# Kernel optimization log

Measured on AMD Instinct MI355X. Metric: run time of the kernel, lower is better.

Reference implementation:

```python
import jax, jax.numpy as jnp
import numpy as np

N = 32768      # nodes
H = 128        # hidden_channels
G = 50         # num_gaussians
F = 128        # num_filters
E = 524288     # edges (avg degree 16)
CUTOFF = 10.0
LOG2 = np.float32(np.log(2.0))


def _lin_init(key, fan_in, fan_out):
    return (jax.random.normal(key, (fan_in, fan_out), jnp.float32) / jnp.sqrt(jnp.float32(fan_in)))


def setup_inputs() -> dict:
    key = jax.random.key(0)
    ks = jax.random.split(key, 12)
    h = jax.random.normal(ks[0], (N, H), jnp.float32)
    pos = jax.random.uniform(ks[1], (N, 3), jnp.float32, minval=0.0, maxval=10.0)
    edge_index = jax.random.randint(ks[2], (2, E), 0, N, jnp.int32)
    virtual_edge_mask = jax.random.randint(ks[3], (E,), 0, 2, jnp.int32) == 1
    return {
        "h": h, "pos": pos,
        "edge_index": edge_index, "virtual_edge_mask": virtual_edge_mask,
        # attn_mlp: Linear(2H+G, H) -> ReLU -> Linear(H, 1)
        "attn_w1": _lin_init(ks[4], 2 * H + G, H), "attn_b1": jnp.zeros((H,), jnp.float32),
        "attn_w2": _lin_init(ks[5], H, 1), "attn_b2": jnp.zeros((1,), jnp.float32),
        # CFConv filter mlp: Linear(G, F) -> ssp -> Linear(F, F)
        "filt_w1": _lin_init(ks[6], G, F), "filt_b1": jnp.zeros((F,), jnp.float32),
        "filt_w2": _lin_init(ks[7], F, F), "filt_b2": jnp.zeros((F,), jnp.float32),
        # CFConv lin1 (no bias), lin2; InteractionBlock output lin
        "lin1_w": _lin_init(ks[8], H, F),
        "lin2_w": _lin_init(ks[9], F, H), "lin2_b": jnp.zeros((H,), jnp.float32),
        "lin_w": _lin_init(ks[10], H, H), "lin_b": jnp.zeros((H,), jnp.float32),
    }


def _ssp(x):  # ShiftedSoftplus
    return jax.nn.softplus(x) - LOG2


def _gaussian_smearing(d):  # [E] -> [E, G]
    offset = jnp.linspace(0.0, CUTOFF, G, dtype=jnp.float32)
    coeff = -0.5 / (offset[1] - offset[0]) ** 2
    return jnp.exp(coeff * (d[:, None] - offset) ** 2)


def _masked_scatter_softmax(score, seg, mask):
    # softmax of score over edges grouped by seg, restricted to mask; 1.0 elsewhere
    neg = jnp.where(mask, score, -jnp.inf)
    m = jax.ops.segment_max(neg, seg, num_segments=N)
    m = jnp.where(jnp.isfinite(m), m, 0.0)
    e = jnp.where(mask, jnp.exp(score - m[seg]), 0.0)
    s = jax.ops.segment_sum(e, seg, num_segments=N)
    return jnp.where(mask, e / (s[seg] + 1e-16), 1.0)


def reference(h, pos, edge_index, virtual_edge_mask,
              attn_w1, attn_b1, attn_w2, attn_b2,
              filt_w1, filt_b1, filt_w2, filt_b2,
              lin1_w, lin2_w, lin2_b, lin_w, lin_b):
    row, col = edge_index[0], edge_index[1]
    d = jnp.linalg.norm(pos[row] - pos[col], axis=-1)          # [E]
    edge_attr = _gaussian_smearing(d)                          # [E, G]

    # attention score over cat(h_i, h_j, edge_attr)
    feat = jnp.concatenate([h[row], h[col], edge_attr], axis=-1)   # [E, 2H+G]
    score = (jax.nn.relu(feat @ attn_w1 + attn_b1) @ attn_w2 + attn_b2)[:, 0]  # [E]
    decay = _masked_scatter_softmax(score, row, virtual_edge_mask)  # [E]
    edge_attr = edge_attr * decay[:, None]

    # PyG SchNet InteractionBlock / CFConv
    C = 0.5 * (jnp.cos(d * jnp.float32(np.pi) / CUTOFF) + 1.0)     # [E]
    W = (_ssp(edge_attr @ filt_w1 + filt_b1) @ filt_w2 + filt_b2) * C[:, None]  # [E, F]
    x = h @ lin1_w                                                  # [N, F]
    msg = x[row] * W                                                # [E, F]
    agg = jax.ops.segment_sum(msg, col, num_segments=N)             # [N, F]
    x = agg @ lin2_w + lin2_b
    h_update = _ssp(x) @ lin_w + lin_b                              # [N, H]
    return h_update, pos
```

## Files before the change

### kernel.cpp

```cpp
#include <hip/hip_runtime.h>

#define NN 32768
#define HH 128
#define GG 50
#define EE 524288

constexpr float GSTEP = 10.0f / 49.0f;
constexpr float GCOEF = -0.5f / (GSTEP * GSTEP);
constexpr float PI_OVER_CUT = 0.31415926535897931f;
constexpr float LOG2F_ = 0.69314718055994531f;
constexpr float LOG2E_ = 1.4426950408889634f;
constexpr float RLOG2E_ = 0.69314718055994531f;
constexpr float GC2 = GCOEF * LOG2E_;

typedef __attribute__((ext_vector_type(8))) short bf16x8;
typedef __attribute__((ext_vector_type(4))) float f32x4;
typedef unsigned short ushort_t;

__device__ __forceinline__ float fast_exp2(float x) {
    float r; asm("v_exp_f32 %0, %1" : "=v"(r) : "v"(x)); return r;
}
__device__ __forceinline__ float fast_log2(float x) {
    float r; asm("v_log_f32 %0, %1" : "=v"(r) : "v"(x)); return r;
}
__device__ __forceinline__ float fexpf(float x) {
    return fast_exp2(x * LOG2E_);
}
__device__ __forceinline__ float sspf(float x) {
    const float p = fast_exp2(x * LOG2E_);
    const float r = RLOG2E_ * fast_log2(1.0f + p) - LOG2F_;
    return (x > 80.0f) ? (x - LOG2F_) : r;
}
__device__ __forceinline__ unsigned fenc(float f) {
    unsigned b = __float_as_uint(f);
    return (b & 0x80000000u) ? ~b : (b | 0x80000000u);
}
__device__ __forceinline__ float fdec(unsigned u) {
    unsigned b = (u & 0x80000000u) ? (u ^ 0x80000000u) : ~u;
    return __uint_as_float(b);
}
__device__ __forceinline__ int get_mask(const void* mp, int mode, int e) {
    if (mode) return ((const unsigned char*)mp)[e] != 0;
    return ((const int*)mp)[e] != 0;
}
__device__ __forceinline__ ushort_t f2bf(float f) {
    unsigned u = __float_as_uint(f);
    return (ushort_t)((u + 0x7FFFu + ((u >> 16) & 1u)) >> 16);
}
__device__ __forceinline__ float bf2f(ushort_t s) { return __uint_as_float(((unsigned)s) << 16); }

__global__ void k_detect(const unsigned char* __restrict__ mb, int* __restrict__ flag) {
    __shared__ int any;
    if (threadIdx.x == 0) any = 0;
    __syncthreads();
    int local = 0;
    for (int i = threadIdx.x; i < 16384; i += blockDim.x)
        if ((i & 3) != 0 && mb[i]) local = 1;
    if (local) atomicOr(&any, 1);
    __syncthreads();
    if (threadIdx.x == 0) *flag = any;
}

__global__ void k_prep_w(const float* __restrict__ filt_w1, const float* __restrict__ filt_w2,
                         const float* __restrict__ attn_w1, const float* __restrict__ lin1_w,
                         const float* __restrict__ lin2_w, const float* __restrict__ lin_w,
                         ushort_t* __restrict__ w1t, ushort_t* __restrict__ w1ct,
                         ushort_t* __restrict__ w2t, ushort_t* __restrict__ wut,
                         ushort_t* __restrict__ wvt, ushort_t* __restrict__ wxt,
                         ushort_t* __restrict__ l2t, ushort_t* __restrict__ lwt)
{
    const int t = blockIdx.x * 256 + threadIdx.x;
    if (t < 8192) {
        const int n = t >> 6, g = t & 63;
        w1t[t] = f2bf((g < GG) ? filt_w1[g * HH + n] : 0.0f);
    } else if (t < 16384) {
        const int i = t - 8192, n = i >> 6, g = i & 63;
        w1ct[i] = f2bf((g < GG) ? attn_w1[(size_t)(256 + g) * HH + n] : 0.0f);
    } else if (t < 32768) {
        const int i = t - 16384, n = i >> 7, k = i & 127;
        w2t[i] = f2bf(filt_w2[k * HH + n]);
    } else if (t < 49152) {
        const int i = t - 32768, n = i >> 7, k = i & 127;
        wut[i] = f2bf(attn_w1[(size_t)k * HH + n]);
    } else if (t < 65536) {
        const int i = t - 49152, n = i >> 7, k = i & 127;
        wvt[i] = f2bf(attn_w1[(size_t)(128 + k) * HH + n]);
    } else if (t < 81920) {
        const int i = t - 65536, n = i >> 7, k = i & 127;
        wxt[i] = f2bf(lin1_w[(size_t)k * HH + n]);
    } else if (t < 98304) {
        const int i = t - 81920, n = i >> 7, k = i & 127;
        l2t[i] = f2bf(lin2_w[(size_t)k * HH + n]);
    } else if (t < 114688) {
        const int i = t - 98304, n = i >> 7, k = i & 127;
        lwt[i] = f2bf(lin_w[(size_t)k * HH + n]);
    }
}

__global__ __launch_bounds__(256, 4) void k_node_proj(
    const float* __restrict__ h,
    const ushort_t* __restrict__ wut, const ushort_t* __restrict__ wvt,
    const ushort_t* __restrict__ wxt,
    ushort_t* __restrict__ ub, ushort_t* __restrict__ vb, ushort_t* __restrict__ xhb)
{
    __shared__ alignas(16) unsigned char smem[32768];
    unsigned char* HB = smem;
    unsigned char* WB = smem + 16384;

    const int tid = threadIdx.x;
    const int n0 = blockIdx.x * 64;
    const int mat = blockIdx.y;
    const ushort_t* __restrict__ wt = (mat == 0) ? wut : (mat == 1 ? wvt : wxt);
    ushort_t* __restrict__ out = (mat == 0) ? ub : (mat == 1 ? vb : xhb);

    for (int p = tid; p < 2048; p += 256) {
        const int row = p >> 5, c4 = p & 31;
        const float4 v = *(const float4*)(h + (size_t)(n0 + row) * HH + c4 * 4);
        uint2 pk = {(unsigned)f2bf(v.x) | ((unsigned)f2bf(v.y) << 16),
                    (unsigned)f2bf(v.z) | ((unsigned)f2bf(v.w) << 16)};
        const int lbyte = row * 256 + c4 * 8;
        *(uint2*)(HB + (lbyte ^ ((row & 7) << 4))) = pk;
    }
    for (int p = tid; p < 1024; p += 256) {
        const int byte = p * 16; const int nl = byte >> 8;
        *(float4*)(WB + (byte ^ ((nl & 7) << 4))) = *(const float4*)((const char*)wt + byte);
    }
    __syncthreads();

    const int lane = tid & 63, wv = tid >> 6, col0 = lane & 15, g4 = lane >> 4;
    const int m = wv * 16 + col0;
    f32x4 acc[8] = {};
#pragma unroll
    for (int hh2 = 0; hh2 < 2; hh2++) {
        if (hh2 == 1) {
            __syncthreads();
            for (int p = tid; p < 1024; p += 256) {
                const int byte = p * 16; const int nl = byte >> 8;
                *(float4*)(WB + (byte ^ ((nl & 7) << 4))) =
                    *(const float4*)((const char*)wt + 16384 + byte);
            }
            __syncthreads();
        }
#pragma unroll
        for (int kk = 0; kk < 4; kk++) {
            const int abyte = m * 256 + kk * 64 + g4 * 16;
            const bf16x8 af = *(const bf16x8*)(HB + (abyte ^ ((m & 7) << 4)));
#pragma unroll
            for (int q = 0; q < 4; q++) {
                const int l = q * 16 + col0;
                const int bbyte = l * 256 + kk * 64 + g4 * 16;
                const bf16x8 bf_ = *(const bf16x8*)(WB + (bbyte ^ ((l & 7) << 4)));
                acc[hh2 * 4 + q] = __builtin_amdgcn_mfma_f32_16x16x32_bf16(af, bf_, acc[hh2 * 4 + q], 0, 0, 0);
            }
        }
    }
#pragma unroll
    for (int f = 0; f < 8; f++) {
        const int col = (f >> 2) * 64 + (f & 3) * 16 + col0;
#pragma unroll
        for (int rg = 0; rg < 4; rg++) {
            const int row = wv * 16 + g4 * 4 + rg;
            out[(size_t)(n0 + row) * HH + col] = f2bf(acc[f][rg]);
        }
    }
}

__global__ __launch_bounds__(256, 4) void k_edge_score(
    const float* __restrict__ pos, const int* __restrict__ ei,
    const void* __restrict__ maskp, const int* __restrict__ flagp,
    const ushort_t* __restrict__ ub, const ushort_t* __restrict__ vb,
    const ushort_t* __restrict__ w1ct, const float* __restrict__ attn_b1,
    const float* __restrict__ attn_w2, const float* __restrict__ attn_b2,
    float* __restrict__ dbuf, float* __restrict__ score, unsigned* __restrict__ menc,
    int* __restrict__ count)
{
    __shared__ alignas(16) unsigned char EA[8192];
    __shared__ alignas(16) unsigned char WC[16384];
    __shared__ float dsh[64];
    __shared__ int rsh[64], csh[64];

    const int tid  = threadIdx.x;
    const int e0   = blockIdx.x * 64;
    const int lane = tid & 63;
    const int wv   = tid >> 6;
    const int col0 = lane & 15;
    const int g4   = lane >> 4;

    if (tid < 64) {
        const int e = e0 + tid;
        const int r = ei[e], c = ei[EE + e];
        rsh[tid] = r; csh[tid] = c;
        atomicAdd(&count[c], 1);
        const float dx = pos[r * 3 + 0] - pos[c * 3 + 0];
        const float dy = pos[r * 3 + 1] - pos[c * 3 + 1];
        const float dz = pos[r * 3 + 2] - pos[c * 3 + 2];
        const float d = sqrtf(dx * dx + dy * dy + dz * dz);
        dsh[tid] = d;
        dbuf[e] = d;
    }
    for (int p = tid; p < 1024; p += 256) {
        const int byte = p * 16;
        const int n = byte >> 7;
        *(float4*)(WC + (byte ^ ((n & 7) << 4))) = *(const float4*)((const char*)w1ct + byte);
    }
    __syncthreads();

    int rrv[4], ccv[4];
#pragma unroll
    for (int rg = 0; rg < 4; rg++) {
        const int e = wv * 16 + g4 * 4 + rg;
        rrv[rg] = rsh[e];
        ccv[rg] = csh[e];
    }
    ushort_t ur[4][8], vr[4][8];
#pragma unroll
    for (int rg = 0; rg < 4; rg++)
#pragma unroll
        for (int n = 0; n < 8; n++) {
            ur[rg][n] = ub[(size_t)rrv[rg] * HH + n * 16 + col0];
            vr[rg][n] = vb[(size_t)ccv[rg] * HH + n * 16 + col0];
        }

    {
        const int e = tid & 63, jg = tid >> 6;
        const float d = dsh[e];
        for (int jj = jg; jj < 8; jj += 4) {
            bf16x8 pk;
#pragma unroll
            for (int b = 0; b < 8; b++) {
                const int g = jj * 8 + b;
                float val = 0.0f;
                if (g < GG) { const float t = d - g * GSTEP; val = fast_exp2(GC2 * t * t); }
                pk[b] = (short)f2bf(val);
            }
            const int byte = e * 128 + jj * 16;
            *(bf16x8*)(EA + (byte ^ ((e & 7) << 4))) = pk;
        }
    }
    float b1v[8], w2v[8];
#pragma unroll
    for (int n = 0; n < 8; n++) {
        b1v[n] = attn_b1[n * 16 + col0];
        w2v[n] = attn_w2[n * 16 + col0];
    }
    __syncthreads();

    const int m = wv * 16 + col0;
    f32x4 acc[8] = {};
#pragma unroll
    for (int kk = 0; kk < 2; kk++) {
        const int abyte = m * 128 + kk * 64 + g4 * 16;
        const bf16x8 af = *(const bf16x8*)(EA + (abyte ^ ((m & 7) << 4)));
#pragma unroll
        for (int n = 0; n < 8; n++) {
            const int l = n * 16 + col0;
            const int bbyte = l * 128 + kk * 64 + g4 * 16;
            const bf16x8 bf_ = *(const bf16x8*)(WC + (bbyte ^ ((l & 7) << 4)));
            acc[n] = __builtin_amdgcn_mfma_f32_16x16x32_bf16(af, bf_, acc[n], 0, 0, 0);
        }
    }

    float pe[4] = {0.0f, 0.0f, 0.0f, 0.0f};
#pragma unroll
    for (int n = 0; n < 8; n++) {
#pragma unroll
        for (int rg = 0; rg < 4; rg++) {
            float z = acc[n][rg] + bf2f(ur[rg][n]) + bf2f(vr[rg][n]) + b1v[n];
            z = fmaxf(z, 0.0f);
            pe[rg] += z * w2v[n];
        }
    }
#pragma unroll
    for (int mask = 1; mask <= 8; mask <<= 1) {
#pragma unroll
        for (int rg = 0; rg < 4; rg++)
            pe[rg] += __shfl_xor(pe[rg], mask, 64);
    }
    if (col0 == 0) {
        const float b2 = attn_b2[0];
        const int mode = *flagp;
#pragma unroll
        for (int rg = 0; rg < 4; rg++) {
            const int e = wv * 16 + g4 * 4 + rg;
            const float s = pe[rg] + b2;
            score[e0 + e] = s;
            if (get_mask(maskp, mode, e0 + e))
                atomicMax(&menc[rsh[e]], fenc(s));
        }
    }
}

__global__ void k_ssum(const float* __restrict__ score, const int* __restrict__ ei,
                       const void* __restrict__ maskp, const int* __restrict__ flagp,
                       const unsigned* __restrict__ menc, float* __restrict__ ssum)
{
    const int e = blockIdx.x * 256 + threadIdx.x;
    if (e >= EE) return;
    const int mode = *flagp;
    if (get_mask(maskp, mode, e)) {
        const int r = ei[e];
        const float m = fdec(menc[r]);
        atomicAdd(&ssum[r], fexpf(score[e] - m));
    }
}

__global__ __launch_bounds__(512) void k_scan(const int* __restrict__ count,
                                              int* __restrict__ cursor)
{
    __shared__ int s[512];
    const int t = threadIdx.x;
    const int base_i = t * 64;
    int sum = 0;
    for (int i = 0; i < 64; i++) sum += count[base_i + i];
    s[t] = sum;
    __syncthreads();
    for (int off = 1; off < 512; off <<= 1) {
        int v = (t >= off) ? s[t - off] : 0;
        __syncthreads();
        s[t] += v;
        __syncthreads();
    }
    int run = s[t] - sum;
    for (int i = 0; i < 64; i++) {
        cursor[base_i + i] = run;
        run += count[base_i + i];
    }
}

__global__ void k_scatter(const int* __restrict__ ei, const void* __restrict__ maskp,
                          const int* __restrict__ flagp,
                          const float* __restrict__ dbuf, const float* __restrict__ score,
                          const unsigned* __restrict__ menc, const float* __restrict__ ssum,
                          int* __restrict__ cursor, uint4* __restrict__ erec)
{
    const int e = blockIdx.x * 256 + threadIdx.x;
    if (e >= EE) return;
    const int r = ei[e], c = ei[EE + e];
    const int pos = atomicAdd(&cursor[c], 1);
    const float d = dbuf[e];
    float dec = 1.0f;
    const int mode = *flagp;
    if (get_mask(maskp, mode, e)) {
        const float m = fdec(menc[r]);
        dec = fexpf(score[e] - m) / (ssum[r] + 1e-16f);
    }
    uint4 rec = {__float_as_uint(d), __float_as_uint(dec),
                 (unsigned)r | ((unsigned)c << 16), 0u};
    erec[pos] = rec;
}

__global__ __launch_bounds__(256, 4) void k_filter_mfma(
    const uint4* __restrict__ erec,
    const ushort_t* __restrict__ w1t, const float* __restrict__ filt_b1,
    const ushort_t* __restrict__ w2t, const float* __restrict__ filt_b2,
    const ushort_t* __restrict__ xhb, float* __restrict__ agg)
{
    __shared__ alignas(16) unsigned char smem[32768];
    unsigned char* EA = smem;
    unsigned char* W1 = smem + 8192;
    unsigned char* T1 = smem + 16384;
    unsigned char* WB = smem;
    float* msgb = (float*)smem;

    __shared__ float dsh[64], decsh[64], Csh[64];
    __shared__ int rsh[64], csh[64];
    __shared__ int shflags;

    const int tid  = threadIdx.x;
    const int e0   = blockIdx.x * 64;
    const int lane = tid & 63;
    const int wv   = tid >> 6;
    const int col0 = lane & 15;
    const int g4   = lane >> 4;

    if (tid < 64) {
        const uint4 rec = erec[e0 + tid];
        const float d = __uint_as_float(rec.x);
        dsh[tid] = d;
        decsh[tid] = __uint_as_float(rec.y);
        rsh[tid] = (int)(rec.z & 0xFFFFu);
        csh[tid] = (int)(rec.z >> 16);
        Csh[tid] = 0.5f * (cosf(d * PI_OVER_CUT) + 1.0f);
    }
    if (tid == 64) {
        const unsigned cf = erec[e0].z >> 16;
        const unsigned cl = erec[e0 + 63].z >> 16;
        int f = 0;
        if (e0 > 0 && (erec[e0 - 1].z >> 16) == cf) f |= 1;
        if (e0 + 64 < EE && (erec[e0 + 64].z >> 16) == cl) f |= 2;
        shflags = f;
    }
    for (int p = tid; p < 512; p += 256) {
        const int byte = p * 16;
        const int n = byte >> 7;
        *(float4*)(W1 + (byte ^ ((n & 7) << 4))) = *(const float4*)((const char*)w1t + byte);
    }
    __syncthreads();

    {
        const int e = tid & 63, jg = tid >> 6;
        const float d = dsh[e], dec = decsh[e];
        for (int jj = jg; jj < 8; jj += 4) {
            bf16x8 pk;
#pragma unroll
            for (int b = 0; b < 8; b++) {
                const int g = jj * 8 + b;
                float val = 0.0f;
                if (g < GG) { const float t = d - g * GSTEP; val = fast_exp2(GC2 * t * t) * dec; }
                pk[b] = (short)f2bf(val);
            }
            const int byte = e * 128 + jj * 16;
            *(bf16x8*)(EA + (byte ^ ((e & 7) << 4))) = pk;
        }
    }
    int rr[4]; float CC[4];
#pragma unroll
    for (int rg = 0; rg < 4; rg++) {
        const int e = wv * 16 + g4 * 4 + rg;
        rr[rg] = rsh[e];
        CC[rg] = Csh[e];
    }
    ushort_t xr[4][8];
#pragma unroll
    for (int rg = 0; rg < 4; rg++)
#pragma unroll
        for (int n = 0; n < 8; n++)
            xr[rg][n] = xhb[(size_t)rr[rg] * HH + n * 16 + col0];
    float b1v[8], b2v[8];
#pragma unroll
    for (int n = 0; n < 8; n++) {
        b1v[n] = filt_b1[n * 16 + col0];
        b2v[n] = filt_b2[n * 16 + col0];
    }
    __syncthreads();

    const int m = wv * 16 + col0;
    f32x4 acc[8] = {};
#pragma unroll
    for (int h = 0; h < 2; h++) {
        if (h == 1) {
            __syncthreads();
            for (int p = tid; p < 512; p += 256) {
                const int byte = p * 16;
                const int n = byte >> 7;
                *(float4*)(W1 + (byte ^ ((n & 7) << 4))) =
                    *(const float4*)((const char*)w1t + 8192 + byte);
            }
            __syncthreads();
        }
#pragma unroll
        for (int kk = 0; kk < 2; kk++) {
            const int abyte = m * 128 + kk * 64 + g4 * 16;
            const bf16x8 af = *(const bf16x8*)(EA + (abyte ^ ((m & 7) << 4)));
#pragma unroll
            for (int q = 0; q < 4; q++) {
                const int l = q * 16 + col0;
                const int bbyte = l * 128 + kk * 64 + g4 * 16;
                const bf16x8 bf_ = *(const bf16x8*)(W1 + (bbyte ^ ((l & 7) << 4)));
                acc[h * 4 + q] = __builtin_amdgcn_mfma_f32_16x16x32_bf16(af, bf_, acc[h * 4 + q], 0, 0, 0);
            }
        }
    }
#pragma unroll
    for (int n = 0; n < 8; n++) {
#pragma unroll
        for (int rg = 0; rg < 4; rg++) {
            const int row = wv * 16 + g4 * 4 + rg;
            const float tv = sspf(acc[n][rg] + b1v[n]);
            const int lbyte = row * 256 + (n * 16 + col0) * 2;
            *(ushort_t*)(T1 + (lbyte ^ ((row & 7) << 4))) = f2bf(tv);
        }
    }
    __syncthreads();

    f32x4 acc2[8] = {};
#pragma unroll
    for (int h = 0; h < 2; h++) {
        for (int p = tid; p < 1024; p += 256) {
            const int byte = p * 16;
            const int nl = byte >> 8;
            *(float4*)(WB + (byte ^ ((nl & 7) << 4))) =
                *(const float4*)((const char*)w2t + h * 16384 + byte);
        }
        __syncthreads();
#pragma unroll
        for (int kk = 0; kk < 4; kk++) {
            const int abyte = m * 256 + kk * 64 + g4 * 16;
            const bf16x8 af = *(const bf16x8*)(T1 + (abyte ^ ((m & 7) << 4)));
#pragma unroll
            for (int q = 0; q < 4; q++) {
                const int l = q * 16 + col0;
                const int bbyte = l * 256 + kk * 64 + g4 * 16;
                const bf16x8 bf_ = *(const bf16x8*)(WB + (bbyte ^ ((l & 7) << 4)));
                acc2[h * 4 + q] = __builtin_amdgcn_mfma_f32_16x16x32_bf16(af, bf_, acc2[h * 4 + q], 0, 0, 0);
            }
        }
        __syncthreads();
    }

#pragma unroll
    for (int n = 0; n < 8; n++) {
        const int col = n * 16 + col0;
#pragma unroll
        for (int rg = 0; rg < 4; rg++) {
            const int e = wv * 16 + g4 * 4 + rg;
            const float Wv = (acc2[n][rg] + b2v[n]) * CC[rg];
            const float xv = __uint_as_float(((unsigned)xr[rg][n]) << 16);
            msgb[e * 128 + ((col + 8 * g4) & 127)] = xv * Wv;
        }
    }
    __syncthreads();

    {
        const int q = tid >> 7;
        const int j = tid & 127;
        const int base = q * 32;
        const int fl = shflags;
        const int cfirst = csh[base], clast = csh[base + 31];
        const int f1 = (q == 0) ? (fl & 1) : (csh[base - 1] == cfirst);
        const int f2 = (q == 1) ? (fl & 2) : (csh[base + 32] == clast);
        float a = msgb[base * 128 + ((j + 8 * ((base >> 2) & 3)) & 127)];
        int cur = cfirst;
        for (int e = base + 1; e < base + 32; e++) {
            const int de = csh[e];
            if (de != cur) {
                if ((cur == cfirst && f1) || (cur == clast && f2))
                    atomicAdd(&agg[(size_t)cur * HH + j], a);
                else
                    agg[(size_t)cur * HH + j] = a;
                a = 0.0f;
                cur = de;
            }
            a += msgb[e * 128 + ((j + 8 * ((e >> 2) & 3)) & 127)];
        }
        if ((cur == cfirst && f1) || (cur == clast && f2))
            atomicAdd(&agg[(size_t)cur * HH + j], a);
        else
            agg[(size_t)cur * HH + j] = a;
    }
}

__global__ __launch_bounds__(256, 4) void k_final(
    const float* __restrict__ agg, const ushort_t* __restrict__ l2t,
    const float* __restrict__ lin2_b, const ushort_t* __restrict__ lwt,
    const float* __restrict__ lin_b, float* __restrict__ out)
{
    __shared__ alignas(16) unsigned char smem[32768];
    unsigned char* AB = smem;
    unsigned char* WB = smem + 16384;
    unsigned char* T1 = smem;

    const int tid = threadIdx.x;
    const int n0 = blockIdx.x * 64;

    for (int p = tid; p < 2048; p += 256) {
        const int row = p >> 5, c4 = p & 31;
        const float4 v = *(const float4*)(agg + (size_t)(n0 + row) * HH + c4 * 4);
        uint2 pk = {(unsigned)f2bf(v.x) | ((unsigned)f2bf(v.y) << 16),
                    (unsigned)f2bf(v.z) | ((unsigned)f2bf(v.w) << 16)};
        const int lbyte = row * 256 + c4 * 8;
        *(uint2*)(AB + (lbyte ^ ((row & 7) << 4))) = pk;
    }
    for (int p = tid; p < 1024; p += 256) {
        const int byte = p * 16; const int nl = byte >> 8;
        *(float4*)(WB + (byte ^ ((nl & 7) << 4))) = *(const float4*)((const char*)l2t + byte);
    }
    __syncthreads();

    const int lane = tid & 63, wv = tid >> 6, col0 = lane & 15, g4 = lane >> 4;
    const int m = wv * 16 + col0;
    float b1v[8], b2v[8];
#pragma unroll
    for (int f = 0; f < 8; f++) {
        const int colf = (f >> 2) * 64 + (f & 3) * 16 + col0;
        b1v[f] = lin2_b[colf];
        b2v[f] = lin_b[colf];
    }

    f32x4 acc[8] = {};
#pragma unroll
    for (int h = 0; h < 2; h++) {
        if (h == 1) {
            __syncthreads();
            for (int p = tid; p < 1024; p += 256) {
                const int byte = p * 16; const int nl = byte >> 8;
                *(float4*)(WB + (byte ^ ((nl & 7) << 4))) =
                    *(const float4*)((const char*)l2t + 16384 + byte);
            }
            __syncthreads();
        }
#pragma unroll
        for (int kk = 0; kk < 4; kk++) {
            const int abyte = m * 256 + kk * 64 + g4 * 16;
            const bf16x8 af = *(const bf16x8*)(AB + (abyte ^ ((m & 7) << 4)));
#pragma unroll
            for (int q = 0; q < 4; q++) {
                const int l = q * 16 + col0;
                const int bbyte = l * 256 + kk * 64 + g4 * 16;
                const bf16x8 bf_ = *(const bf16x8*)(WB + (bbyte ^ ((l & 7) << 4)));
                acc[h * 4 + q] = __builtin_amdgcn_mfma_f32_16x16x32_bf16(af, bf_, acc[h * 4 + q], 0, 0, 0);
            }
        }
    }
    __syncthreads();

#pragma unroll
    for (int f = 0; f < 8; f++) {
        const int colf = (f >> 2) * 64 + (f & 3) * 16 + col0;
#pragma unroll
        for (int rg = 0; rg < 4; rg++) {
            const int row = wv * 16 + g4 * 4 + rg;
            const float tv = sspf(acc[f][rg] + b1v[f]);
            const int lbyte = row * 256 + colf * 2;
            *(ushort_t*)(T1 + (lbyte ^ ((row & 7) << 4))) = f2bf(tv);
        }
    }
    for (int p = tid; p < 1024; p += 256) {
        const int byte = p * 16; const int nl = byte >> 8;
        *(float4*)(WB + (byte ^ ((nl & 7) << 4))) = *(const float4*)((const char*)lwt + byte);
    }
    __syncthreads();

    f32x4 acc2[8] = {};
#pragma unroll
    for (int h = 0; h < 2; h++) {
        if (h == 1) {
            __syncthreads();
            for (int p = tid; p < 1024; p += 256) {
                const int byte = p * 16; const int nl = byte >> 8;
                *(float4*)(WB + (byte ^ ((nl & 7) << 4))) =
                    *(const float4*)((const char*)lwt + 16384 + byte);
            }
            __syncthreads();
        }
#pragma unroll
        for (int kk = 0; kk < 4; kk++) {
            const int abyte = m * 256 + kk * 64 + g4 * 16;
            const bf16x8 af = *(const bf16x8*)(T1 + (abyte ^ ((m & 7) << 4)));
#pragma unroll
            for (int q = 0; q < 4; q++) {
                const int l = q * 16 + col0;
                const int bbyte = l * 256 + kk * 64 + g4 * 16;
                const bf16x8 bf_ = *(const bf16x8*)(WB + (bbyte ^ ((l & 7) << 4)));
                acc2[h * 4 + q] = __builtin_amdgcn_mfma_f32_16x16x32_bf16(af, bf_, acc2[h * 4 + q], 0, 0, 0);
            }
        }
    }
#pragma unroll
    for (int f = 0; f < 8; f++) {
        const int colf = (f >> 2) * 64 + (f & 3) * 16 + col0;
#pragma unroll
        for (int rg = 0; rg < 4; rg++) {
            const int row = wv * 16 + g4 * 4 + rg;
            out[(size_t)(n0 + row) * HH + colf] = acc2[f][rg] + b2v[f];
        }
    }
}

__global__ void k_copy_pos(const float* __restrict__ pos, float* __restrict__ out) {
    const int i = blockIdx.x * 256 + threadIdx.x;
    if (i < NN * 3) out[i] = pos[i];
}

extern "C" void kernel_launch(void* const* d_in, const int* in_sizes, int n_in,
                              void* d_out, int out_size, void* d_ws, size_t ws_size,
                              hipStream_t stream)
{
    const float* h       = (const float*)d_in[0];
    const float* pos     = (const float*)d_in[1];
    const int*   ei      = (const int*)d_in[2];
    const void*  maskp   = d_in[3];
    const float* attn_w1 = (const float*)d_in[4];
    const float* attn_b1 = (const float*)d_in[5];
    const float* attn_w2 = (const float*)d_in[6];
    const float* attn_b2 = (const float*)d_in[7];
    const float* filt_w1 = (const float*)d_in[8];
    const float* filt_b1 = (const float*)d_in[9];
    const float* filt_w2 = (const float*)d_in[10];
    const float* filt_b2 = (const float*)d_in[11];
    const float* lin1_w  = (const float*)d_in[12];
    const float* lin2_w  = (const float*)d_in[13];
    const float* lin2_b  = (const float*)d_in[14];
    const float* lin_w   = (const float*)d_in[15];
    const float* lin_b   = (const float*)d_in[16];

    char* p = (char*)d_ws;
    auto alloc = [&](size_t bytes) { char* r = p; p += (bytes + 255) & ~(size_t)255; return r; };

    ushort_t* ub    = (ushort_t*)alloc((size_t)NN * HH * 2);
    ushort_t* vb    = (ushort_t*)alloc((size_t)NN * HH * 2);
    ushort_t* xhb   = (ushort_t*)alloc((size_t)NN * HH * 2);
    float*    dbuf  = (float*)alloc((size_t)EE * 4);
    float*    score = (float*)alloc((size_t)EE * 4);
    unsigned* menc  = (unsigned*)alloc((size_t)NN * 4);
    float*    ssum  = (float*)alloc((size_t)NN * 4);
    int*      count = (int*)alloc((size_t)NN * 4);
    int*      cursor= (int*)alloc((size_t)NN * 4);
    float*    agg   = (float*)alloc((size_t)NN * HH * 4);
    int*      flag  = (int*)alloc(4);
    uint4*    erec  = (uint4*)alloc((size_t)EE * 16);
    ushort_t* w1t   = (ushort_t*)alloc((size_t)128 * 64 * 2);
    ushort_t* w1ct  = (ushort_t*)alloc((size_t)128 * 64 * 2);
    ushort_t* w2t   = (ushort_t*)alloc((size_t)128 * 128 * 2);
    ushort_t* wut   = (ushort_t*)alloc((size_t)128 * 128 * 2);
    ushort_t* wvt   = (ushort_t*)alloc((size_t)128 * 128 * 2);
    ushort_t* wxt   = (ushort_t*)alloc((size_t)128 * 128 * 2);
    ushort_t* l2t   = (ushort_t*)alloc((size_t)128 * 128 * 2);
    ushort_t* lwt   = (ushort_t*)alloc((size_t)128 * 128 * 2);

    float* out_h   = (float*)d_out;
    float* out_pos = out_h + (size_t)NN * HH;

    hipMemsetAsync(menc, 0, (size_t)3 * NN * 4, stream);

    k_detect<<<1, 256, 0, stream>>>((const unsigned char*)maskp, flag);
    k_prep_w<<<448, 256, 0, stream>>>(filt_w1, filt_w2, attn_w1, lin1_w, lin2_w, lin_w,
                                      w1t, w1ct, w2t, wut, wvt, wxt, l2t, lwt);
    k_node_proj<<<dim3(NN / 64, 3), 256, 0, stream>>>(h, wut, wvt, wxt, ub, vb, xhb);
    k_edge_score<<<EE / 64, 256, 0, stream>>>(pos, ei, maskp, flag, ub, vb,
                                              w1ct, attn_b1, attn_w2, attn_b2,
                                              dbuf, score, menc, count);
    k_ssum<<<EE / 256, 256, 0, stream>>>(score, ei, maskp, flag, menc, ssum);
    k_scan<<<1, 512, 0, stream>>>(count, cursor);
    k_scatter<<<EE / 256, 256, 0, stream>>>(ei, maskp, flag, dbuf, score, menc, ssum,
                                            cursor, erec);

    hipMemsetAsync(agg, 0, (size_t)NN * HH * sizeof(float), stream);
    k_filter_mfma<<<EE / 64, 256, 0, stream>>>(erec, w1t, filt_b1, w2t, filt_b2, xhb, agg);

    k_final<<<NN / 64, 256, 0, stream>>>(agg, l2t, lin2_b, lwt, lin_b, out_h);
    k_copy_pos<<<(NN * 3 + 255) / 256, 256, 0, stream>>>(pos, out_pos);
}
```

Measured before the change: 350.7 us.

## Compact masked edges so attention scoring runs only on virtual edges

Adds a compaction kernel that counts in-degree and, using a global atomic counter, builds a list of masked (virtual) edges. The attention-score MFMA kernel and the softmax-sum kernel then process only those edges, with blocks past the count exiting early. Scores of unmasked edges are never used, so this skips about half of the attention MLP work. Edge distances are now recomputed in the scatter kernel instead of stored, which removes the distance buffer. The cost is an extra kernel pass, a global atomic per masked edge, and compacted records in nondeterministic order, which changes gather locality.

```diff
diff --git a/kernel.cpp b/kernel.cpp
--- a/kernel.cpp
+++ b/kernel.cpp
@@ -165,38 +165,63 @@
     }
 }
 
+__global__ void k_compact(const int* __restrict__ ei, const void* __restrict__ maskp,
+                          const int* __restrict__ flagp,
+                          int* __restrict__ count, int* __restrict__ mcount,
+                          uint2* __restrict__ mrec)
+{
+    const int e = blockIdx.x * 256 + threadIdx.x;
+    if (e >= EE) return;
+    const int r = ei[e], c = ei[EE + e];
+    atomicAdd(&count[c], 1);
+    const int mode = *flagp;
+    if (get_mask(maskp, mode, e)) {
+        const int pos = atomicAdd(mcount, 1);
+        uint2 rec = {(unsigned)e, (unsigned)r | ((unsigned)c << 16)};
+        mrec[pos] = rec;
+    }
+}
+
 __global__ __launch_bounds__(256, 4) void k_edge_score(
-    const float* __restrict__ pos, const int* __restrict__ ei,
-    const void* __restrict__ maskp, const int* __restrict__ flagp,
+    const float* __restrict__ pos, const uint2* __restrict__ mrec,
+    const int* __restrict__ mcount,
     const ushort_t* __restrict__ ub, const ushort_t* __restrict__ vb,
     const ushort_t* __restrict__ w1ct, const float* __restrict__ attn_b1,
     const float* __restrict__ attn_w2, const float* __restrict__ attn_b2,
-    float* __restrict__ dbuf, float* __restrict__ score, unsigned* __restrict__ menc,
-    int* __restrict__ count)
+    float* __restrict__ score, unsigned* __restrict__ menc)
 {
     __shared__ alignas(16) unsigned char EA[8192];
     __shared__ alignas(16) unsigned char WC[16384];
     __shared__ float dsh[64];
-    __shared__ int rsh[64], csh[64];
+    __shared__ int rsh[64], csh[64], esh[64];
+    __shared__ int Em_s;
 
     const int tid  = threadIdx.x;
-    const int e0   = blockIdx.x * 64;
+    if (tid == 0) Em_s = *mcount;
+    __syncthreads();
+    const int Em = Em_s;
+    const int base = blockIdx.x * 64;
+    if (base >= Em) return;
+
     const int lane = tid & 63;
     const int wv   = tid >> 6;
     const int col0 = lane & 15;
     const int g4   = lane >> 4;
 
     if (tid < 64) {
-        const int e = e0 + tid;
-        const int r = ei[e], c = ei[EE + e];
-        rsh[tid] = r; csh[tid] = c;
-        atomicAdd(&count[c], 1);
+        const int slot = base + tid;
+        int e = -1, r = 0, c = 0;
+        if (slot < Em) {
+            const uint2 rec = mrec[slot];
+            e = (int)rec.x;
+            r = (int)(rec.y & 0xFFFFu);
+            c = (int)(rec.y >> 16);
+        }
+        esh[tid] = e; rsh[tid] = r; csh[tid] = c;
         const float dx = pos[r * 3 + 0] - pos[c * 3 + 0];
         const float dy = pos[r * 3 + 1] - pos[c * 3 + 1];
         const float dz = pos[r * 3 + 2] - pos[c * 3 + 2];
-        const float d = sqrtf(dx * dx + dy * dy + dz * dz);
-        dsh[tid] = d;
-        dbuf[e] = d;
+        dsh[tid] = sqrtf(dx * dx + dy * dy + dz * dz);
     }
     for (int p = tid; p < 1024; p += 256) {
         const int byte = p * 16;
@@ -278,30 +303,29 @@
     }
     if (col0 == 0) {
         const float b2 = attn_b2[0];
-        const int mode = *flagp;
 #pragma unroll
         for (int rg = 0; rg < 4; rg++) {
-            const int e = wv * 16 + g4 * 4 + rg;
-            const float s = pe[rg] + b2;
-            score[e0 + e] = s;
-            if (get_mask(maskp, mode, e0 + e))
-                atomicMax(&menc[rsh[e]], fenc(s));
-        }
-    }
-}
-
-__global__ void k_ssum(const float* __restrict__ score, const int* __restrict__ ei,
-                       const void* __restrict__ maskp, const int* __restrict__ flagp,
-                       const unsigned* __restrict__ menc, float* __restrict__ ssum)
-{
-    const int e = blockIdx.x * 256 + threadIdx.x;
-    if (e >= EE) return;
-    const int mode = *flagp;
-    if (get_mask(maskp, mode, e)) {
-        const int r = ei[e];
-        const float m = fdec(menc[r]);
-        atomicAdd(&ssum[r], fexpf(score[e] - m));
-    }
+            const int le = wv * 16 + g4 * 4 + rg;
+            const int e = esh[le];
+            if (e >= 0) {
+                const float s = pe[rg] + b2;
+                score[e] = s;
+                atomicMax(&menc[rsh[le]], fenc(s));
+            }
+        }
+    }
+}
+
+__global__ void k_ssum(const uint2* __restrict__ mrec, const int* __restrict__ mcount,
+                       const float* __restrict__ score, const unsigned* __restrict__ menc,
+                       float* __restrict__ ssum)
+{
+    const int slot = blockIdx.x * 256 + threadIdx.x;
+    if (slot >= *mcount) return;
+    const uint2 rec = mrec[slot];
+    const int e = (int)rec.x;
+    const int r = (int)(rec.y & 0xFFFFu);
+    atomicAdd(&ssum[r], fexpf(score[e] - fdec(menc[r])));
 }
 
 __global__ __launch_bounds__(512) void k_scan(const int* __restrict__ count,
@@ -328,16 +352,19 @@
 }
 
 __global__ void k_scatter(const int* __restrict__ ei, const void* __restrict__ maskp,
-                          const int* __restrict__ flagp,
-                          const float* __restrict__ dbuf, const float* __restrict__ score,
+                          const int* __restrict__ flagp, const float* __restrict__ pos,
+                          const float* __restrict__ score,
                           const unsigned* __restrict__ menc, const float* __restrict__ ssum,
                           int* __restrict__ cursor, uint4* __restrict__ erec)
 {
     const int e = blockIdx.x * 256 + threadIdx.x;
     if (e >= EE) return;
     const int r = ei[e], c = ei[EE + e];
-    const int pos = atomicAdd(&cursor[c], 1);
-    const float d = dbuf[e];
+    const int p = atomicAdd(&cursor[c], 1);
+    const float dx = pos[r * 3 + 0] - pos[c * 3 + 0];
+    const float dy = pos[r * 3 + 1] - pos[c * 3 + 1];
+    const float dz = pos[r * 3 + 2] - pos[c * 3 + 2];
+    const float d = sqrtf(dx * dx + dy * dy + dz * dz);
     float dec = 1.0f;
     const int mode = *flagp;
     if (get_mask(maskp, mode, e)) {
@@ -346,7 +373,7 @@
     }
     uint4 rec = {__float_as_uint(d), __float_as_uint(dec),
                  (unsigned)r | ((unsigned)c << 16), 0u};
-    erec[pos] = rec;
+    erec[p] = rec;
 }
 
 __global__ __launch_bounds__(256, 4) void k_filter_mfma(
@@ -690,14 +717,15 @@
     ushort_t* ub    = (ushort_t*)alloc((size_t)NN * HH * 2);
     ushort_t* vb    = (ushort_t*)alloc((size_t)NN * HH * 2);
     ushort_t* xhb   = (ushort_t*)alloc((size_t)NN * HH * 2);
-    float*    dbuf  = (float*)alloc((size_t)EE * 4);
     float*    score = (float*)alloc((size_t)EE * 4);
     unsigned* menc  = (unsigned*)alloc((size_t)NN * 4);
     float*    ssum  = (float*)alloc((size_t)NN * 4);
     int*      count = (int*)alloc((size_t)NN * 4);
+    int*      mcount= (int*)alloc(4);
     int*      cursor= (int*)alloc((size_t)NN * 4);
     float*    agg   = (float*)alloc((size_t)NN * HH * 4);
     int*      flag  = (int*)alloc(4);
+    uint2*    mrec  = (uint2*)alloc((size_t)EE * 8);
     uint4*    erec  = (uint4*)alloc((size_t)EE * 16);
     ushort_t* w1t   = (ushort_t*)alloc((size_t)128 * 64 * 2);
     ushort_t* w1ct  = (ushort_t*)alloc((size_t)128 * 64 * 2);
@@ -711,18 +739,19 @@
     float* out_h   = (float*)d_out;
     float* out_pos = out_h + (size_t)NN * HH;
 
-    hipMemsetAsync(menc, 0, (size_t)3 * NN * 4, stream);
+    hipMemsetAsync(menc, 0, (size_t)3 * NN * 4 + 256, stream);
 
     k_detect<<<1, 256, 0, stream>>>((const unsigned char*)maskp, flag);
     k_prep_w<<<448, 256, 0, stream>>>(filt_w1, filt_w2, attn_w1, lin1_w, lin2_w, lin_w,
                                       w1t, w1ct, w2t, wut, wvt, wxt, l2t, lwt);
     k_node_proj<<<dim3(NN / 64, 3), 256, 0, stream>>>(h, wut, wvt, wxt, ub, vb, xhb);
-    k_edge_score<<<EE / 64, 256, 0, stream>>>(pos, ei, maskp, flag, ub, vb,
+    k_compact<<<EE / 256, 256, 0, stream>>>(ei, maskp, flag, count, mcount, mrec);
+    k_edge_score<<<EE / 64, 256, 0, stream>>>(pos, mrec, mcount, ub, vb,
                                               w1ct, attn_b1, attn_w2, attn_b2,
-                                              dbuf, score, menc, count);
-    k_ssum<<<EE / 256, 256, 0, stream>>>(score, ei, maskp, flag, menc, ssum);
+                                              score, menc);
+    k_ssum<<<EE / 256, 256, 0, stream>>>(mrec, mcount, score, menc, ssum);
     k_scan<<<1, 512, 0, stream>>>(count, cursor);
-    k_scatter<<<EE / 256, 256, 0, stream>>>(ei, maskp, flag, dbuf, score, menc, ssum,
+    k_scatter<<<EE / 256, 256, 0, stream>>>(ei, maskp, flag, pos, score, menc, ssum,
                                             cursor, erec);
 
     hipMemsetAsync(agg, 0, (size_t)NN * HH * sizeof(float), stream);
```

Result: slower. 402.8 us (+14.9%).
